# Performance work log

Measured on AMD Instinct MI355X. Metric: run time of the kernel, lower is better.

The kernel has to match this reference:

```python
import math
import jax, jax.numpy as jnp
import numpy as np

B, N, D = 2, 768, 512
H = 8
DK = D // H
BETA_NOT = 0.5
EPS = 1e-6


def setup_inputs() -> dict:
    key = jax.random.key(0)
    ks = jax.random.split(key, 8)
    s = 0.02
    return {
        "x": jax.random.normal(ks[0], (B, N, D), dtype=jnp.float32),
        "qkv1_w": jax.random.normal(ks[1], (D, 3 * D), dtype=jnp.float32) * s,
        "qkv2_w": jax.random.normal(ks[2], (D, 3 * D), dtype=jnp.float32) * s,
        "proj_w": jax.random.normal(ks[3], (D, D), dtype=jnp.float32) * s,
        "conv1_w": jax.random.normal(ks[4], (16, 6), dtype=jnp.float32) * 0.3,
        "conv1_b": jax.random.normal(ks[5], (16,), dtype=jnp.float32) * 0.1,
        "conv2_w": jax.random.normal(ks[6], (4, 16), dtype=jnp.float32) * 0.3,
        "conv2_b": jnp.full((4,), -5.0, dtype=jnp.float32),
        "chain_logit": jnp.asarray(-2.0, dtype=jnp.float32),
    }


def _qkv(x, w):
    b, n, d = x.shape
    qkv = (x @ w).reshape(b, n, 3, H, DK).transpose(2, 0, 3, 1, 4)  # [3,B,h,N,dk]
    return qkv[0], qkv[1], qkv[2]


def reference(x, qkv1_w, qkv2_w, proj_w, conv1_w, conv1_b, conv2_w, conv2_b, chain_logit):
    scale = 1.0 / math.sqrt(DK)
    q1, k1, v1 = _qkv(x, qkv1_w)
    q2, k2, v2 = _qkv(x, qkv2_w)

    S1 = jnp.einsum("bhnd,bhmd->bhnm", q1, k1) * scale  # [B,h,N,N]
    S2 = jnp.einsum("bhnd,bhmd->bhnm", q2, k2) * scale
    A1 = jax.nn.softmax(S1, axis=-1)
    A2 = jax.nn.softmax(S2, axis=-1)

    C_right = jnp.einsum("bhnk,bhkm->bhnm", A1, A2)
    C_left = jnp.einsum("bhnk,bhkm->bhnm", A2, A1)
    Cr = jnp.log(C_right + EPS)
    Cl = jnp.log(C_left + EPS)

    # 6-channel edge feature map [B,h,6,N,N]
    feat = jnp.stack(
        [S1, S2, jnp.swapaxes(S1, -1, -2), jnp.swapaxes(S2, -1, -2), Cr, Cl], axis=2
    )
    # 1x1 convs == per-pixel channel mixing
    hid = jnp.einsum("bhcnm,oc->bhonm", feat, conv1_w) + conv1_b[None, None, :, None, None]
    hid = jax.nn.gelu(hid, approximate=True)  # tanh-approx GELU
    gates = jax.nn.sigmoid(
        jnp.einsum("bhcnm,oc->bhonm", hid, conv2_w) + conv2_b[None, None, :, None, None]
    )
    g_and, g_or, g_not, g_chain = gates[:, :, 0], gates[:, :, 1], gates[:, :, 2], gates[:, :, 3]

    Smix = (
        S1
        + g_and * S2  # g_and * (S1 + S2 - S1)
        + g_or * (jnp.logaddexp(S1, S2) - S1)
        - g_not * (BETA_NOT * S2)
        + g_chain * Cr
    )
    A = jax.nn.softmax(Smix, axis=-1)

    y_base = jnp.einsum("bhnm,bhmd->bhnd", A, v1)
    transport = jnp.einsum("bhnm,bhmd->bhnd", A2, v2)
    y_chain = jnp.einsum("bhnm,bhmd->bhnd", A1, transport)
    w = jax.nn.sigmoid(chain_logit)
    y = y_base + w * y_chain

    y = jnp.swapaxes(y, 1, 2).reshape(x.shape[0], x.shape[1], D)  # [B,N,D]
    return y @ proj_w
```

## Files before the change

kernel.cpp:

```cpp
#include <hip/hip_runtime.h>
#include <hip/hip_bf16.h>
#include <math.h>

typedef __hip_bfloat16 bf16;
typedef __attribute__((ext_vector_type(8))) short short8;
typedef __attribute__((ext_vector_type(4))) float f32x4;
typedef __attribute__((ext_vector_type(2))) float f32x2;
#define DEVINL __device__ __forceinline__

constexpr int Bc  = 2;
constexpr int Nc  = 768;
constexpr int Dc  = 512;
constexpr int Hc  = 8;
constexpr int DKc = 64;
constexpr int BHc = Bc * Hc;
constexpr float SCALE    = 0.125f;
constexpr float EPSF     = 1e-6f;
constexpr float BETA_NOT = 0.5f;

DEVINL float ldf(const float* p, long i) { return p[i]; }
DEVINL float ldf(const bf16* p, long i) { return __bfloat162float(p[i]); }
DEVINL void stf(float* p, long i, float v) { p[i] = v; }
DEVINL void stf(bf16* p, long i, float v) { p[i] = __float2bfloat16(v); }

DEVINL float sigf(float x) { return __fdividef(1.f, 1.f + __expf(-x)); }

DEVINL f32x2 fma2(f32x2 a, f32x2 b, f32x2 c) { return __builtin_elementwise_fma(a, b, c); }
DEVINL f32x2 splat2(float x) { return (f32x2){x, x}; }
DEVINL float vexp2(float x) { float r; asm("v_exp_f32 %0, %1" : "=v"(r) : "v"(x)); return r; }
DEVINL float vrcp(float x)  { float r; asm("v_rcp_f32 %0, %1" : "=v"(r) : "v"(x)); return r; }
DEVINL float vlog2(float x) { float r; asm("v_log_f32 %0, %1" : "=v"(r) : "v"(x)); return r; }

DEVINL void gl_lds16(const void* g, void* l) {
    __builtin_amdgcn_global_load_lds(
        (const __attribute__((address_space(1))) void*)g,
        (__attribute__((address_space(3))) void*)l, 16, 0, 0);
}

DEVINL int sniff_is_fp32(const void* xraw) {
    const uint4* p4 = (const uint4*)xraw;
    float mx = 0.f;
#pragma unroll
    for (int j = 0; j < 16; ++j) {
        const uint4 u = p4[j];
        const unsigned w[4] = {u.x, u.y, u.z, u.w};
#pragma unroll
        for (int t = 0; t < 4; ++t) {
            mx = fmaxf(mx, fabsf(__uint_as_float((w[t] & 0xffffu) << 16)));
            mx = fmaxf(mx, fabsf(__uint_as_float(w[t] & 0xffff0000u)));
        }
    }
    return mx > 1000.f ? 1 : 0;
}

DEVINL float cvt_elem(const void* s, long j, int is32) {
    return is32 ? ((const float*)s)[j]
                : __bfloat162float(((const bf16*)s)[j]);
}

__global__ __launch_bounds__(256) void convert_tr(
    const void* x, const void* w1, const void* w2, const void* pw,
    const void* c1w, const void* c1b, const void* c2w, const void* c2b,
    const void* ch,
    bf16* xb, bf16* w1t, bf16* w2t, bf16* pwt, float* smallf)
{
    __shared__ unsigned short tile[64][68];
    __shared__ int is32s;
    if (threadIdx.x == 0) is32s = sniff_is_fp32(x);
    __syncthreads();
    const int is32 = is32s;
    const int t = blockIdx.x;
    const int tid = threadIdx.x;

    if (t < 448) {
        const void* src; bf16* dst; int R, C, bx, by;
        if (t < 192)      { src = w1; dst = w1t; R = Dc; C = 3 * Dc;
                            bx = t % 24;         by = t / 24; }
        else if (t < 384) { src = w2; dst = w2t; R = Dc; C = 3 * Dc;
                            bx = (t - 192) % 24; by = (t - 192) / 24; }
        else              { src = pw; dst = pwt; R = Dc; C = Dc;
                            bx = (t - 384) % 8;  by = (t - 384) / 8; }
        const int r0 = by * 64, c0 = bx * 64;
        const int lr = tid >> 4, lc4 = (tid & 15) * 4;
#pragma unroll
        for (int i = 0; i < 4; ++i) {
            const int r = lr + i * 16;
            const long base = (long)(r0 + r) * C + c0 + lc4;
            unsigned short v[4];
            if (is32) {
                const float4 f = *(const float4*)&((const float*)src)[base];
                const bf16 b0 = __float2bfloat16(f.x);
                const bf16 b1 = __float2bfloat16(f.y);
                const bf16 b2 = __float2bfloat16(f.z);
                const bf16 b3 = __float2bfloat16(f.w);
                v[0] = *(const unsigned short*)&b0;
                v[1] = *(const unsigned short*)&b1;
                v[2] = *(const unsigned short*)&b2;
                v[3] = *(const unsigned short*)&b3;
            } else {
                *(uint2*)v = *(const uint2*)&((const unsigned short*)src)[base];
            }
            *(uint2*)&tile[r][lc4] = *(const uint2*)v;
        }
        __syncthreads();
#pragma unroll
        for (int i = 0; i < 4; ++i) {
            const int r = lr + i * 16;
            unsigned short v[4];
#pragma unroll
            for (int j = 0; j < 4; ++j) v[j] = tile[lc4 + j][r];
            *(uint2*)&((unsigned short*)dst)[(long)(c0 + r) * R + r0 + lc4] =
                *(const uint2*)v;
        }
    } else if (t < 832) {
        const long i0 = (long)(t - 448) * 2048 + tid * 8;
        if (is32) {
            const float4 a = *(const float4*)&((const float*)x)[i0];
            const float4 b = *(const float4*)&((const float*)x)[i0 + 4];
            const float f[8] = {a.x, a.y, a.z, a.w, b.x, b.y, b.z, b.w};
            unsigned short o[8];
#pragma unroll
            for (int j = 0; j < 8; ++j) {
                const bf16 bb = __float2bfloat16(f[j]);
                o[j] = *(const unsigned short*)&bb;
            }
            *(uint4*)&((unsigned short*)xb)[i0] = *(const uint4*)o;
        } else {
            *(uint4*)&((unsigned short*)xb)[i0] =
                *(const uint4*)&((const unsigned short*)x)[i0];
        }
    } else {
#pragma unroll
        for (int base = 0; base < 512; base += 256) {
            const int i = base + tid;
            if (i < 384) {
                const int u = i / 24, k = i % 24;
                float v = 0.f;
                if (k < 12)      v = cvt_elem(c1w, u * 6 + (k >> 1), is32);
                else if (k < 14) v = cvt_elem(c1b, u, is32);
                else if (k >= 16) { const int o = (k - 16) >> 1;
                                    v = cvt_elem(c2w, o * 16 + u, is32); }
                smallf[i] = v;
            } else if (i < 392) smallf[i] = cvt_elem(c2b, (i - 384) >> 1, is32);
            else if (i < 394) smallf[i] = cvt_elem(ch, 0, is32);
            else smallf[i] = 0.f;
        }
    }
}

__global__ __launch_bounds__(256) void fill_sentinel(unsigned short* o) {
    const long i = (long)blockIdx.x * 256 + threadIdx.x;
    if (i < (long)Bc * Nc * Dc) o[i] = 0x40E0;
}

__global__ __launch_bounds__(256) void sgemm_softmax(
    const bf16* __restrict__ qg, const bf16* __restrict__ kg,
    float* __restrict__ Sg, bf16* __restrict__ Ag_, bf16* __restrict__ Atg)
{
    __shared__ unsigned short Bsm[256 * 72];
    __shared__ unsigned short Asm16[16 * 72];
    __shared__ float red[4][16];

    const int wg  = blockIdx.x;
    const int xcd = wg & 7, tt = wg >> 3;
    const int z   = xcd + 8 * (tt / 48);
    const int by  = tt % 48;
    const long MAT = (long)Nc * Nc;

    const bf16* Q  = qg + (long)z * (Nc * DKc) + (long)(by * 16) * DKc;
    const bf16* Km = kg + (long)z * (Nc * DKc);
    float* S  = Sg  + (long)z * MAT + (long)(by * 16) * Nc;
    bf16*  A  = Ag_ + (long)z * MAT + (long)(by * 16) * Nc;
    bf16*  At = Atg + (long)z * MAT;

    const int tid  = threadIdx.x;
    const int wv   = tid >> 6;
    const int lane = tid & 63;
    const int q    = lane >> 4;
    const int ln   = lane & 15;
    const int sr   = tid >> 3, k8 = tid & 7;

    if (tid < 128) {
        const int row = tid >> 3, kk = tid & 7;
        *(uint4*)&Asm16[row * 72 + kk * 8] = *(const uint4*)&Q[row * 64 + kk * 8];
    }

    f32x4 acc[12];
#pragma unroll
    for (int j = 0; j < 12; ++j) acc[j] = (f32x4){0.f, 0.f, 0.f, 0.f};

    for (int c = 0; c < 3; ++c) {
        __syncthreads();
#pragma unroll
        for (int i = 0; i < 8; ++i) {
            const int row = sr + i * 32;
            *(uint4*)&Bsm[row * 72 + k8 * 8] =
                *(const uint4*)&Km[(long)(c * 256 + row) * 64 + k8 * 8];
        }
        __syncthreads();
#pragma unroll
        for (int kc = 0; kc < 2; ++kc) {
            const short8 af = *(const short8*)&Asm16[ln * 72 + kc * 32 + q * 8];
#pragma unroll
            for (int t = 0; t < 4; ++t) {
                const int nl = wv * 64 + t * 16 + ln;
                const short8 bfr = *(const short8*)&Bsm[nl * 72 + kc * 32 + q * 8];
                acc[c * 4 + t] = __builtin_amdgcn_mfma_f32_16x16x32_bf16(
                    af, bfr, acc[c * 4 + t], 0, 0, 0);
            }
        }
    }

    float mrow[4] = {-1e30f, -1e30f, -1e30f, -1e30f};
#pragma unroll
    for (int j = 0; j < 12; ++j) {
        const int c = j >> 2, t = j & 3;
        const int col = c * 256 + wv * 64 + t * 16 + ln;
#pragma unroll
        for (int r = 0; r < 4; ++r) {
            const float v = acc[j][r] * SCALE;
            acc[j][r] = v;
            S[(long)(q * 4 + r) * Nc + col] = v;
            mrow[r] = fmaxf(mrow[r], v);
        }
    }
#pragma unroll
    for (int off = 8; off > 0; off >>= 1)
#pragma unroll
        for (int r = 0; r < 4; ++r)
            mrow[r] = fmaxf(mrow[r], __shfl_xor(mrow[r], off, 16));
    if (ln == 0)
#pragma unroll
        for (int r = 0; r < 4; ++r) red[wv][q * 4 + r] = mrow[r];
    __syncthreads();
    float m4[4];
#pragma unroll
    for (int r = 0; r < 4; ++r)
        m4[r] = fmaxf(fmaxf(red[0][q * 4 + r], red[1][q * 4 + r]),
                      fmaxf(red[2][q * 4 + r], red[3][q * 4 + r]));
    __syncthreads();

    float srow[4] = {0.f, 0.f, 0.f, 0.f};
#pragma unroll
    for (int j = 0; j < 12; ++j)
#pragma unroll
        for (int r = 0; r < 4; ++r) {
            const float e = __expf(acc[j][r] - m4[r]);
            acc[j][r] = e;
            srow[r] += e;
        }
#pragma unroll
    for (int off = 8; off > 0; off >>= 1)
#pragma unroll
        for (int r = 0; r < 4; ++r)
            srow[r] += __shfl_xor(srow[r], off, 16);
    if (ln == 0)
#pragma unroll
        for (int r = 0; r < 4; ++r) red[wv][q * 4 + r] = srow[r];
    __syncthreads();
    float inv[4];
#pragma unroll
    for (int r = 0; r < 4; ++r)
        inv[r] = 1.f / fmaxf(red[0][q * 4 + r] + red[1][q * 4 + r] +
                             red[2][q * 4 + r] + red[3][q * 4 + r], 1e-30f);

    unsigned short* ATl = Bsm;
#pragma unroll
    for (int j = 0; j < 12; ++j) {
        const int c = j >> 2, t = j & 3;
        const int col = c * 256 + wv * 64 + t * 16 + ln;
#pragma unroll
        for (int r = 0; r < 4; ++r) {
            const bf16 b = __float2bfloat16(acc[j][r] * inv[r]);
            const unsigned short u = *(const unsigned short*)&b;
            A[(long)(q * 4 + r) * Nc + col] = *(const bf16*)&u;
            ATl[col * 20 + q * 4 + r] = u;
        }
    }
    __syncthreads();
#pragma unroll
    for (int s = 0; s < 3; ++s) {
        const int m = tid + s * 256;
        uint2 v0 = *(const uint2*)&ATl[m * 20 + 0];
        uint2 v1 = *(const uint2*)&ATl[m * 20 + 4];
        uint2 v2 = *(const uint2*)&ATl[m * 20 + 8];
        uint2 v3 = *(const uint2*)&ATl[m * 20 + 12];
        unsigned short* d = (unsigned short*)&At[(long)m * Nc + by * 16];
        *(uint2*)&d[0]  = v0;
        *(uint2*)&d[4]  = v1;
        *(uint2*)&d[8]  = v2;
        *(uint2*)&d[12] = v3;
    }
}

template <int EPI, typename TC, int XORB = 0, int XCDSWZ = 0, int RAW = 0>
__global__ __launch_bounds__(256) void gemm_nt_mfma(
    const bf16* __restrict__ Ag, const bf16* __restrict__ Btg,
    TC* __restrict__ Cg, bf16* __restrict__ Craw, int M, int N, int K,
    long sA, long sB, long sC, float alpha)
{
    __shared__ unsigned short Asm[2 * 128 * 32];
    __shared__ unsigned short Bsm[2 * 128 * 32];
    constexpr int BUF = 128 * 32;

    int bx, by, bz;
    if (XCDSWZ) {
        const int wg = blockIdx.x;
        const int xcd = wg & 7, t = wg >> 3;
        bz = xcd + 8 * (t / 36);
        const int tile = t % 36;
        bx = tile % 6; by = tile / 6;
    } else { bx = blockIdx.x; by = blockIdx.y; bz = blockIdx.z; }

    const int tid  = threadIdx.x;
    const int wv   = tid >> 6;
    const int lane = tid & 63;
    const int q    = lane >> 4;
    const int ln   = lane & 15;
    const int wm   = wv & 1;
    const int wn   = wv >> 1;

    const int zb = XORB ? (bz ^ 16) : bz;
    const bf16* A  = Ag  + (long)bz * sA + (long)(by * 128) * K;
    const bf16* Bt = Btg + (long)zb * sB + (long)(bx * 128) * K;
    TC*         C  = Cg  + (long)bz * sC;

    const int sr = lane >> 2, sc = lane & 3;
    const int scs = sc ^ (sr & 3);
    const bf16* gA0 = A  + (long)(wv * 32 + sr)      * K + scs * 8;
    const bf16* gA1 = A  + (long)(wv * 32 + 16 + sr) * K + scs * 8;
    const bf16* gB0 = Bt + (long)(wv * 32 + sr)      * K + scs * 8;
    const bf16* gB1 = Bt + (long)(wv * 32 + 16 + sr) * K + scs * 8;
    unsigned short* lA0 = &Asm[(wv * 32)      * 32];
    unsigned short* lA1 = &Asm[(wv * 32 + 16) * 32];
    unsigned short* lB0 = &Bsm[(wv * 32)      * 32];
    unsigned short* lB1 = &Bsm[(wv * 32 + 16) * 32];

    f32x4 acc[4][4];
#pragma unroll
    for (int i = 0; i < 4; ++i)
#pragma unroll
        for (int j = 0; j < 4; ++j)
            acc[i][j] = (f32x4){0.f, 0.f, 0.f, 0.f};

    const int qs = (q ^ (ln & 3)) * 8;

    gl_lds16(gA0, lA0);
    gl_lds16(gA1, lA1);
    gl_lds16(gB0, lB0);
    gl_lds16(gB1, lB1);
    __syncthreads();

    int cur = 0;
    for (int k0 = 0; k0 < K; k0 += 32) {
        const int nxt = cur ^ 1;
        if (k0 + 32 < K) {
            const int no = nxt * BUF;
            gl_lds16(gA0 + k0 + 32, lA0 + no);
            gl_lds16(gA1 + k0 + 32, lA1 + no);
            gl_lds16(gB0 + k0 + 32, lB0 + no);
            gl_lds16(gB1 + k0 + 32, lB1 + no);
        }

        const unsigned short* Ac = &Asm[cur * BUF];
        const unsigned short* Bc = &Bsm[cur * BUF];
        short8 af[4], bfr[4];
#pragma unroll
        for (int mt = 0; mt < 4; ++mt) {
            int m = wm * 64 + mt * 16 + ln;
            af[mt] = *(const short8*)&Ac[m * 32 + qs];
        }
#pragma unroll
        for (int nt = 0; nt < 4; ++nt) {
            int n = wn * 64 + nt * 16 + ln;
            bfr[nt] = *(const short8*)&Bc[n * 32 + qs];
        }
#pragma unroll
        for (int mt = 0; mt < 4; ++mt)
#pragma unroll
            for (int nt = 0; nt < 4; ++nt)
                acc[mt][nt] = __builtin_amdgcn_mfma_f32_16x16x32_bf16(
                    af[mt], bfr[nt], acc[mt][nt], 0, 0, 0);

        __syncthreads();
        cur = nxt;
    }

#pragma unroll
    for (int mt = 0; mt < 4; ++mt) {
#pragma unroll
        for (int nt = 0; nt < 4; ++nt) {
            const int col = bx * 128 + wn * 64 + nt * 16 + ln;
            const int rowb = by * 128 + wm * 64 + mt * 16 + q * 4;
#pragma unroll
            for (int r = 0; r < 4; ++r) {
                float vraw = acc[mt][nt][r] * alpha;
                if (RAW) {
                    if (bz < 16)
                        Craw[(long)bz * M * N + (long)(rowb + r) * N + col] =
                            __float2bfloat16(vraw);
                }
                float v = vraw;
                if (EPI == 1) v = __logf(fmaxf(v, 0.f) + EPSF);
                stf(C, (long)(rowb + r) * N + col, v);
            }
        }
    }
}

__global__ __launch_bounds__(256) void qkv_mfma64(
    const bf16* __restrict__ X,
    const bf16* __restrict__ w1t, const bf16* __restrict__ w2t,
    bf16* __restrict__ q1, bf16* __restrict__ k1, bf16* __restrict__ v1t,
    bf16* __restrict__ q2, bf16* __restrict__ k2, bf16* __restrict__ v2t)
{
    constexpr int K = Dc;
    __shared__ unsigned short Asm[2 * 64 * 32];
    __shared__ unsigned short Bsm[2 * 128 * 32];
    constexpr int ABUF = 64 * 32, BBUF = 128 * 32;

    const int tid  = threadIdx.x;
    const int wv   = tid >> 6;
    const int lane = tid & 63;
    const int q    = lane >> 4;
    const int ln   = lane & 15;
    const int wm   = wv & 1;
    const int wn   = wv >> 1;
    const int set  = blockIdx.z;

    const bf16* Wt = set ? w2t : w1t;
    bf16* Q  = set ? q2 : q1;
    bf16* Ko = set ? k2 : k1;
    bf16* Vt = set ? v2t : v1t;

    const bf16* A  = X  + (long)(blockIdx.y * 64) * K;
    const bf16* Bt = Wt + (long)(blockIdx.x * 128) * K;

    const int sr = lane >> 2, sc = lane & 3;
    const int scs = sc ^ (sr & 3);
    const bf16* gA0 = A  + (long)(wv * 16 + sr)      * K + scs * 8;
    const bf16* gB0 = Bt + (long)(wv * 32 + sr)      * K + scs * 8;
    const bf16* gB1 = Bt + (long)(wv * 32 + 16 + sr) * K + scs * 8;
    unsigned short* lA0 = &Asm[(wv * 16)      * 32];
    unsigned short* lB0 = &Bsm[(wv * 32)      * 32];
    unsigned short* lB1 = &Bsm[(wv * 32 + 16) * 32];

    f32x4 acc[2][4];
#pragma unroll
    for (int i = 0; i < 2; ++i)
#pragma unroll
        for (int j = 0; j < 4; ++j)
            acc[i][j] = (f32x4){0.f, 0.f, 0.f, 0.f};

    const int qs = (q ^ (ln & 3)) * 8;

    gl_lds16(gA0, lA0);
    gl_lds16(gB0, lB0);
    gl_lds16(gB1, lB1);
    __syncthreads();

    int cur = 0;
    for (int k0 = 0; k0 < K; k0 += 32) {
        const int nxt = cur ^ 1;
        if (k0 + 32 < K) {
            gl_lds16(gA0 + k0 + 32, lA0 + nxt * ABUF);
            gl_lds16(gB0 + k0 + 32, lB0 + nxt * BBUF);
            gl_lds16(gB1 + k0 + 32, lB1 + nxt * BBUF);
        }

        const unsigned short* Ac = &Asm[cur * ABUF];
        const unsigned short* Bc = &Bsm[cur * BBUF];
        short8 af[2], bfr[4];
#pragma unroll
        for (int mt = 0; mt < 2; ++mt) {
            int m = wm * 32 + mt * 16 + ln;
            af[mt] = *(const short8*)&Ac[m * 32 + qs];
        }
#pragma unroll
        for (int nt = 0; nt < 4; ++nt) {
            int n = wn * 64 + nt * 16 + ln;
            bfr[nt] = *(const short8*)&Bc[n * 32 + qs];
        }
#pragma unroll
        for (int mt = 0; mt < 2; ++mt)
#pragma unroll
            for (int nt = 0; nt < 4; ++nt)
                acc[mt][nt] = __builtin_amdgcn_mfma_f32_16x16x32_bf16(
                    af[mt], bfr[nt], acc[mt][nt], 0, 0, 0);

        __syncthreads();
        cur = nxt;
    }

#pragma unroll
    for (int mt = 0; mt < 2; ++mt) {
#pragma unroll
        for (int nt = 0; nt < 4; ++nt) {
            const int col  = blockIdx.x * 128 + wn * 64 + nt * 16 + ln;
            const int rowb = blockIdx.y * 64 + wm * 32 + mt * 16 + q * 4;
            const int t = col >> 9;
            const int h = (col >> 6) & 7;
            const int dk = col & 63;
            if (t == 2) {
                const int b = rowb >= Nc ? 1 : 0;
                const int n = rowb - b * Nc;
                unsigned short o[4];
#pragma unroll
                for (int r = 0; r < 4; ++r) {
                    const bf16 bb = __float2bfloat16(acc[mt][nt][r]);
                    o[r] = *(const unsigned short*)&bb;
                }
                unsigned short* d = (unsigned short*)Vt +
                    (((long)b * Hc + h) * DKc + dk) * Nc + n;
                *(uint2*)d = *(const uint2*)o;
            } else {
                bf16* dst = (t == 0) ? Q : Ko;
#pragma unroll
                for (int r = 0; r < 4; ++r) {
                    const int row = rowb + r;
                    const int b = row >= Nc ? 1 : 0;
                    const int n = row - b * Nc;
                    dst[(((long)b * Hc + h) * Nc + n) * DKc + dk] =
                        __float2bfloat16(acc[mt][nt][r]);
                }
            }
        }
    }
}

struct N64Acc { f32x4 acc[2][4]; };

template <typename DUMMY = void>
DEVINL void n64_core(const bf16* A, const bf16* Bt, int K,
                     unsigned short* Asm, unsigned short* Bsm, N64Acc& R)
{
    const int tid  = threadIdx.x;
    const int wave = tid >> 6;
    const int lane = tid & 63;
    const int q    = lane >> 4;
    const int ln   = lane & 15;

    const int sr = tid >> 3, k8 = tid & 7;
    const bf16* pa[4];
    const bf16* pb[2];
    int wa[4], wb[2];
#pragma unroll
    for (int i = 0; i < 4; ++i) {
        pa[i] = A + (long)(sr + i * 32) * K + k8 * 8;
        wa[i] = (sr + i * 32) * 72 + k8 * 8;
    }
#pragma unroll
    for (int i = 0; i < 2; ++i) {
        pb[i] = Bt + (long)(sr + i * 32) * K + k8 * 8;
        wb[i] = (sr + i * 32) * 72 + k8 * 8;
    }

#pragma unroll
    for (int i = 0; i < 2; ++i)
#pragma unroll
        for (int j = 0; j < 4; ++j)
            R.acc[i][j] = (f32x4){0.f, 0.f, 0.f, 0.f};

    for (int k0 = 0; k0 < K; k0 += 64) {
        uint4 va[4], vb[2];
#pragma unroll
        for (int i = 0; i < 4; ++i) va[i] = *(const uint4*)(pa[i] + k0);
#pragma unroll
        for (int i = 0; i < 2; ++i) vb[i] = *(const uint4*)(pb[i] + k0);
        __syncthreads();
#pragma unroll
        for (int i = 0; i < 4; ++i) *(uint4*)&Asm[wa[i]] = va[i];
#pragma unroll
        for (int i = 0; i < 2; ++i) *(uint4*)&Bsm[wb[i]] = vb[i];
        __syncthreads();

#pragma unroll
        for (int kc = 0; kc < 2; ++kc) {
            short8 af[2], bfr[4];
#pragma unroll
            for (int mt = 0; mt < 2; ++mt) {
                int m = wave * 32 + mt * 16 + ln;
                af[mt] = *(const short8*)&Asm[m * 72 + kc * 32 + q * 8];
            }
#pragma unroll
            for (int nt = 0; nt < 4; ++nt) {
                int n = nt * 16 + ln;
                bfr[nt] = *(const short8*)&Bsm[n * 72 + kc * 32 + q * 8];
            }
#pragma unroll
            for (int mt = 0; mt < 2; ++mt)
#pragma unroll
                for (int nt = 0; nt < 4; ++nt)
                    R.acc[mt][nt] = __builtin_amdgcn_mfma_f32_16x16x32_bf16(
                        af[mt], bfr[nt], R.acc[mt][nt], 0, 0, 0);
        }
    }
}

struct N64hAcc { f32x4 acc[4]; };

template <typename DUMMY = void>
DEVINL void n64h_core(const bf16* A, const bf16* Bt, int K,
                      unsigned short* Asm, unsigned short* Bsm, N64hAcc& R)
{
    const int tid  = threadIdx.x;
    const int wave = tid >> 6;
    const int lane = tid & 63;
    const int q    = lane >> 4;
    const int ln   = lane & 15;

    const int sr = tid >> 3, k8 = tid & 7;
    const bf16* pa[2];
    const bf16* pb[2];
    int wa[2], wb[2];
#pragma unroll
    for (int i = 0; i < 2; ++i) {
        pa[i] = A  + (long)(sr + i * 32) * K + k8 * 8;
        wa[i] = (sr + i * 32) * 72 + k8 * 8;
        pb[i] = Bt + (long)(sr + i * 32) * K + k8 * 8;
        wb[i] = wa[i];
    }

#pragma unroll
    for (int j = 0; j < 4; ++j)
        R.acc[j] = (f32x4){0.f, 0.f, 0.f, 0.f};

    for (int k0 = 0; k0 < K; k0 += 64) {
        uint4 va[2], vb[2];
#pragma unroll
        for (int i = 0; i < 2; ++i) va[i] = *(const uint4*)(pa[i] + k0);
#pragma unroll
        for (int i = 0; i < 2; ++i) vb[i] = *(const uint4*)(pb[i] + k0);
        __syncthreads();
#pragma unroll
        for (int i = 0; i < 2; ++i) *(uint4*)&Asm[wa[i]] = va[i];
#pragma unroll
        for (int i = 0; i < 2; ++i) *(uint4*)&Bsm[wb[i]] = vb[i];
        __syncthreads();

#pragma unroll
        for (int kc = 0; kc < 2; ++kc) {
            short8 af;
            af = *(const short8*)&Asm[(wave * 16 + ln) * 72 + kc * 32 + q * 8];
            short8 bfr[4];
#pragma unroll
            for (int nt = 0; nt < 4; ++nt) {
                int n = nt * 16 + ln;
                bfr[nt] = *(const short8*)&Bsm[n * 72 + kc * 32 + q * 8];
            }
#pragma unroll
            for (int nt = 0; nt < 4; ++nt)
                R.acc[nt] = __builtin_amdgcn_mfma_f32_16x16x32_bf16(
                    af, bfr[nt], R.acc[nt], 0, 0, 0);
        }
    }
}

__global__ __launch_bounds__(256) void gemm_n64_pair(
    const bf16* __restrict__ A0g, const bf16* __restrict__ B0g, bf16* __restrict__ C0tg,
    const bf16* __restrict__ A1g, const bf16* __restrict__ B1g, bf16* __restrict__ C1g,
    int M, int K, long sA, long sB, long sC)
{
    __shared__ unsigned short Asm[128 * 72];
    __shared__ unsigned short Bsm[64 * 72];

    const int zz = blockIdx.z & 15;
    const int second = blockIdx.z >> 4;
    const bf16* A  = (second ? A1g : A0g) + (long)zz * sA + (long)(blockIdx.y * 128) * K;
    const bf16* Bt = (second ? B1g : B0g) + (long)zz * sB;

    N64Acc R;
    n64_core(A, Bt, K, Asm, Bsm, R);

    const int tid = threadIdx.x;
    const int wave = tid >> 6, lane = tid & 63, q = lane >> 4, ln = lane & 15;

    if (second) {
        bf16* C = C1g + (long)zz * sC;
#pragma unroll
        for (int mt = 0; mt < 2; ++mt) {
#pragma unroll
            for (int nt = 0; nt < 4; ++nt) {
                const int col  = nt * 16 + ln;
                const int rowb = blockIdx.y * 128 + wave * 32 + mt * 16 + q * 4;
#pragma unroll
                for (int r = 0; r < 4; ++r)
                    C[(long)(rowb + r) * 64 + col] = __float2bfloat16(R.acc[mt][nt][r]);
            }
        }
    } else {
        __syncthreads();
#pragma unroll
        for (int mt = 0; mt < 2; ++mt) {
#pragma unroll
            for (int nt = 0; nt < 4; ++nt) {
                const int col = nt * 16 + ln;
                const int rwb = wave * 32 + mt * 16 + q * 4;
#pragma unroll
                for (int r = 0; r < 4; ++r)
                    *(bf16*)&Asm[col * 136 + rwb + r] = __float2bfloat16(R.acc[mt][nt][r]);
            }
        }
        __syncthreads();
        bf16* Ct = C0tg + (long)zz * sC;
        const int dk  = tid >> 2;
        const int nc0 = (tid & 3) * 32;
        const int gn0 = blockIdx.y * 128;
#pragma unroll
        for (int c8 = 0; c8 < 4; ++c8) {
            uint4 v = *(const uint4*)&Asm[dk * 136 + nc0 + c8 * 8];
            *(uint4*)&Ct[(long)dk * Nc + gn0 + nc0 + c8 * 8] = v;
        }
    }
}

__global__ __launch_bounds__(256) void gemm_n64_both_h(
    const bf16* __restrict__ Ab, const bf16* __restrict__ v1t,
    const bf16* __restrict__ Craw, const bf16* __restrict__ v2t,
    const float* __restrict__ smallf, bf16* __restrict__ yc,
    int K, long sA, long sB)
{
    __shared__ unsigned short Asm[64 * 72];
    __shared__ unsigned short Bsm[64 * 72];

    const int bh = blockIdx.z;
    const long arow = (long)(blockIdx.y * 64) * K;

    N64hAcc R1;
    n64h_core(Ab + (long)bh * sA + arow, v1t + (long)bh * sB, K, Asm, Bsm, R1);
    N64hAcc R2;
    n64h_core(Craw + (long)bh * sA + arow, v2t + (long)bh * sB, K, Asm, Bsm, R2);

    const float w = sigf(smallf[392]);
    const int b = bh >> 3, h = bh & 7;

    const int tid = threadIdx.x;
    const int wave = tid >> 6, lane = tid & 63, q = lane >> 4, ln = lane & 15;
#pragma unroll
    for (int nt = 0; nt < 4; ++nt) {
        const int col  = nt * 16 + ln;
        const int rowb = blockIdx.y * 64 + wave * 16 + q * 4;
#pragma unroll
        for (int r = 0; r < 4; ++r) {
            const int n = rowb + r;
            yc[((long)(b * Nc + n)) * Dc + h * DKc + col] =
                __float2bfloat16(R1.acc[nt][r] + w * R2.acc[nt][r]);
        }
    }
}

__global__ __launch_bounds__(256) void gemm_n64_combine(
    const bf16* __restrict__ A1b, const bf16* __restrict__ trt,
    const bf16* __restrict__ yb1, const float* __restrict__ smallf,
    bf16* __restrict__ yc, int M, int K, long sA, long sB)
{
    __shared__ unsigned short Asm[128 * 72];
    __shared__ unsigned short Bsm[64 * 72];

    const int bh = blockIdx.z;
    const bf16* A  = A1b + (long)bh * sA + (long)(blockIdx.y * 128) * K;
    const bf16* Bt = trt + (long)bh * sB;

    N64Acc R;
    n64_core(A, Bt, K, Asm, Bsm, R);

    const float w = sigf(smallf[392]);
    const int b = bh >> 3, h = bh & 7;
    const long yb1base = (long)bh * Nc * DKc;

    const int tid = threadIdx.x;
    const int wave = tid >> 6, lane = tid & 63, q = lane >> 4, ln = lane & 15;
#pragma unroll
    for (int mt = 0; mt < 2; ++mt) {
#pragma unroll
        for (int nt = 0; nt < 4; ++nt) {
            const int col  = nt * 16 + ln;
            const int rowb = blockIdx.y * 128 + wave * 32 + mt * 16 + q * 4;
#pragma unroll
            for (int r = 0; r < 4; ++r) {
                const int n = rowb + r;
                const float base = __bfloat162float(yb1[yb1base + (long)n * 64 + col]);
                yc[((long)(b * Nc + n)) * Dc + h * DKc + col] =
                    __float2bfloat16(base + w * R.acc[mt][nt][r]);
            }
        }
    }
}

__global__ __launch_bounds__(256) void gemm_n64_yb(
    const bf16* __restrict__ Ag, const bf16* __restrict__ Btg,
    bf16* __restrict__ Cg, int M, int K, long sA, long sB, long sC)
{
    __shared__ unsigned short Asm[128 * 72];
    __shared__ unsigned short Bsm[64 * 72];

    const int zz = blockIdx.z;
    const bf16* A  = Ag + (long)zz * sA + (long)(blockIdx.y * 128) * K;
    const bf16* Bt = Btg + (long)zz * sB;

    N64Acc R;
    n64_core(A, Bt, K, Asm, Bsm, R);

    bf16* C = Cg + (long)zz * sC;
    const int tid = threadIdx.x;
    const int wave = tid >> 6, lane = tid & 63, q = lane >> 4, ln = lane & 15;
#pragma unroll
    for (int mt = 0; mt < 2; ++mt) {
#pragma unroll
        for (int nt = 0; nt < 4; ++nt) {
            const int col  = nt * 16 + ln;
            const int rowb = blockIdx.y * 128 + wave * 32 + mt * 16 + q * 4;
#pragma unroll
            for (int r = 0; r < 4; ++r)
                C[(long)(rowb + r) * 64 + col] = __float2bfloat16(R.acc[mt][nt][r]);
        }
    }
}

__global__ __launch_bounds__(256) void softmax_rows_w(
    const float* __restrict__ src, bf16* __restrict__ dst)
{
    const int wid  = threadIdx.x >> 6;
    const int lane = threadIdx.x & 63;
    const long row = (long)blockIdx.x * 4 + wid;
    const float* s = src + row * Nc;

    float4 v[3];
#pragma unroll
    for (int i = 0; i < 3; ++i)
        v[i] = *(const float4*)&s[i * 256 + lane * 4];

    float m = -1e30f;
#pragma unroll
    for (int i = 0; i < 3; ++i)
        m = fmaxf(m, fmaxf(fmaxf(v[i].x, v[i].y), fmaxf(v[i].z, v[i].w)));
#pragma unroll
    for (int off = 32; off > 0; off >>= 1)
        m = fmaxf(m, __shfl_xor(m, off, 64));

    float e[12];
    float sum = 0.f;
#pragma unroll
    for (int i = 0; i < 3; ++i) {
        e[i * 4 + 0] = __expf(v[i].x - m);
        e[i * 4 + 1] = __expf(v[i].y - m);
        e[i * 4 + 2] = __expf(v[i].z - m);
        e[i * 4 + 3] = __expf(v[i].w - m);
        sum += e[i * 4 + 0] + e[i * 4 + 1] + e[i * 4 + 2] + e[i * 4 + 3];
    }
#pragma unroll
    for (int off = 32; off > 0; off >>= 1)
        sum += __shfl_xor(sum, off, 64);

    const float inv = 1.f / fmaxf(sum, 1e-30f);
    unsigned short* d = (unsigned short*)dst + row * Nc;
#pragma unroll
    for (int i = 0; i < 3; ++i) {
        unsigned short o[4];
#pragma unroll
        for (int j = 0; j < 4; ++j) {
            const bf16 b = __float2bfloat16(e[i * 4 + j] * inv);
            o[j] = *(const unsigned short*)&b;
        }
        *(uint2*)&d[i * 256 + lane * 4] = *(const uint2*)o;
    }
}

__global__ __launch_bounds__(256) void gates_smix(
    const float* __restrict__ S1g, const float* __restrict__ S2g,
    const bf16* __restrict__ Crg, const bf16* __restrict__ Clg,
    float* __restrict__ Smixg, const float* __restrict__ smallf)
{
    __shared__ float t1t[32][17], t2t[32][17];

    const long mat = (long)blockIdx.z * Nc * Nc;
    const float* S1 = S1g + mat;
    const float* S2 = S2g + mat;
    const unsigned short* Cr = (const unsigned short*)Crg + mat;
    const unsigned short* Cl = (const unsigned short*)Clg + mat;
    float* Smix = Smixg + mat;

    const int tid = threadIdx.x;

    const int n0 = blockIdx.y * 16, m0 = blockIdx.x * 32;
    {
        const int r = tid >> 3, c2 = (tid & 7) * 2;
        const float2 a = *(const float2*)&S1[(long)(m0 + r) * Nc + n0 + c2];
        const float2 b = *(const float2*)&S2[(long)(m0 + r) * Nc + n0 + c2];
        t1t[r][c2] = a.x; t1t[r][c2 + 1] = a.y;
        t2t[r][c2] = b.x; t2t[r][c2 + 1] = b.y;
    }
    __syncthreads();

    const int tx = tid & 15, ty = tid >> 4;
    const int n = n0 + ty;
    const long idx = (long)n * Nc + m0 + tx * 2;

    const float2 s1v = *(const float2*)&S1[idx];
    const float2 s2v = *(const float2*)&S2[idx];
    const unsigned cru = *(const unsigned*)&Cr[idx];
    const unsigned clu = *(const unsigned*)&Cl[idx];

    const f32x2 s1a = {s1v.x, s1v.y};
    const f32x2 s2a = {s2v.x, s2v.y};
    const f32x2 cra = {__uint_as_float((cru & 0xffffu) << 16),
                       __uint_as_float(cru & 0xffff0000u)};
    const f32x2 cla = {__uint_as_float((clu & 0xffffu) << 16),
                       __uint_as_float(clu & 0xffff0000u)};
    const f32x2 s1t = {t1t[tx * 2][ty], t1t[tx * 2 + 1][ty]};
    const f32x2 s2t = {t2t[tx * 2][ty], t2t[tx * 2 + 1][ty]};

    f32x2 g0 = *(const f32x2*)&smallf[384];
    f32x2 g1 = *(const f32x2*)&smallf[386];
    f32x2 g2 = *(const f32x2*)&smallf[388];
    f32x2 g3 = *(const f32x2*)&smallf[390];

    const f32x2 gc1  = splat2(-2.30220902f);
    const f32x2 gc3  = splat2(-0.10294357f);
    const f32x2 one2 = splat2(1.f);

#pragma unroll
    for (int u = 0; u < 16; ++u) {
        const f32x2* cw = (const f32x2*)&smallf[u * 24];
        f32x2 h = cw[6];
        h = fma2(s1a, cw[0], h);
        h = fma2(s2a, cw[1], h);
        h = fma2(s1t, cw[2], h);
        h = fma2(s2t, cw[3], h);
        h = fma2(cra, cw[4], h);
        h = fma2(cla, cw[5], h);
        const f32x2 hh = h * h;
        const f32x2 z2 = h * fma2(hh, gc3, gc1);
        f32x2 e;  e[0]  = vexp2(z2[0]); e[1]  = vexp2(z2[1]);
        const f32x2 d = one2 + e;
        f32x2 rc; rc[0] = vrcp(d[0]);   rc[1] = vrcp(d[1]);
        const f32x2 hid = h * rc;
        g0 = fma2(hid, cw[8],  g0);
        g1 = fma2(hid, cw[9],  g1);
        g2 = fma2(hid, cw[10], g2);
        g3 = fma2(hid, cw[11], g3);
    }

    const f32x2 nl2e = splat2(-1.44269504f);
    const f32x2 ln2v = splat2(0.69314718f);
    auto sig2 = [&](f32x2 x) -> f32x2 {
        const f32x2 t = x * nl2e;
        f32x2 e;  e[0] = vexp2(t[0]); e[1] = vexp2(t[1]);
        const f32x2 d = one2 + e;
        f32x2 r;  r[0] = vrcp(d[0]);  r[1] = vrcp(d[1]);
        return r;
    };
    const f32x2 ga2 = sig2(g0);
    const f32x2 go2 = sig2(g1);
    const f32x2 gn2 = sig2(g2);
    const f32x2 gc2 = sig2(g3);

    const f32x2 dd = s1a - s2a;
    f32x2 ad; ad[0] = fabsf(dd[0]); ad[1] = fabsf(dd[1]);
    const f32x2 t2 = ad * nl2e;
    f32x2 ee; ee[0] = vexp2(t2[0]); ee[1] = vexp2(t2[1]);
    const f32x2 lp = one2 + ee;
    f32x2 lg; lg[0] = vlog2(lp[0]); lg[1] = vlog2(lp[1]);
    const f32x2 mx2 = __builtin_elementwise_max(s1a, s2a);
    const f32x2 lae = fma2(lg, ln2v, mx2);

    f32x2 o2 = s1a;
    o2 = fma2(ga2, s2a, o2);
    o2 = fma2(go2, lae - s1a, o2);
    o2 = fma2(gn2, s2a * splat2(-BETA_NOT), o2);
    o2 = fma2(gc2, cra, o2);
    *(float2*)&Smix[idx] = (float2){o2[0], o2[1]};
}

__global__ __launch_bounds__(256) void proj_n64h(
    const bf16* __restrict__ yc, const bf16* __restrict__ pwt,
    const void* __restrict__ xraw, void* __restrict__ out)
{
    constexpr int K = Dc;
    constexpr int N = Dc;
    __shared__ unsigned short Asm[64 * 72];
    __shared__ unsigned short Bsm[64 * 72];
    __shared__ int is32s;
    if (threadIdx.x == 0) is32s = sniff_is_fp32(xraw);

    const bf16* A  = yc  + (long)(blockIdx.y * 64) * K;
    const bf16* Bt = pwt + (long)(blockIdx.x * 64) * K;

    N64hAcc R;
    n64h_core(A, Bt, K, Asm, Bsm, R);

    const int is32 = is32s;
    const int tid = threadIdx.x;
    const int wave = tid >> 6, lane = tid & 63, q = lane >> 4, ln = lane & 15;
#pragma unroll
    for (int nt = 0; nt < 4; ++nt) {
        const int col  = blockIdx.x * 64 + nt * 16 + ln;
        const int rowb = blockIdx.y * 64 + wave * 16 + q * 4;
#pragma unroll
        for (int r = 0; r < 4; ++r) {
            const long o = (long)(rowb + r) * N + col;
            if (is32) ((float*)out)[o] = R.acc[nt][r];
            else      ((bf16*)out)[o] = __float2bfloat16(R.acc[nt][r]);
        }
    }
}

extern "C" void kernel_launch(void* const* d_in, const int* in_sizes, int n_in,
                              void* d_out, int out_size, void* d_ws, size_t ws_size,
                              hipStream_t stream)
{
    const size_t HD   = (size_t)BHc * Nc * DKc;
    const size_t HDh  = HD / 2;
    const size_t MAT  = (size_t)Nc * Nc;
    const size_t MATS = (size_t)BHc * MAT;
    const long   HSTR = (long)Nc * DKc;

    float* ws = (float*)d_ws;
    size_t off = 0;
    auto alloc = [&](size_t n) { float* p = ws + off; off += n; return p; };

    bf16* xb  = (bf16*)alloc(HDh);
    bf16* w1t = (bf16*)alloc(HDh);
    bf16* w2t = (bf16*)alloc(HDh);
    bf16* pwt = (bf16*)alloc((size_t)Dc * Dc / 2);
    float* smallf = alloc(512);
    bf16* q1b = (bf16*)alloc(HDh); bf16* q2b = (bf16*)alloc(HDh);
    bf16* k1b = (bf16*)alloc(HDh); bf16* k2b = (bf16*)alloc(HDh);
    bf16* v1t = (bf16*)alloc(HDh); bf16* v2t = (bf16*)alloc(HDh);
    bf16* trt = (bf16*)alloc(HDh);
    float* S1   = alloc(MATS);
    float* S2   = alloc(MATS);
    float* Smix = alloc(MATS);
    bf16* A1b = (bf16*)alloc(MATS / 2);
    bf16* A2b = (bf16*)alloc(MATS / 2);
    bf16* Crb = (bf16*)alloc(MATS / 2);
    bf16* Clb = (bf16*)alloc(MATS / 2);
    bf16* yb1 = (bf16*)alloc(HDh);
    bf16* yc  = (bf16*)alloc(HDh);

    const size_t NEED_BASE = off * sizeof(float);
    bf16* Crawb = (bf16*)alloc(MATS / 2);
    const size_t NEED_A = off * sizeof(float);
    const int pathA = ws_size >= NEED_A;

    bf16* A1tb = (bf16*)Smix;
    bf16* A2tb = ((bf16*)Smix) + MATS;
    bf16* Ab   = (bf16*)S1;

    if (ws_size < NEED_BASE) {
        fill_sentinel<<<dim3(3072), 256, 0, stream>>>((unsigned short*)d_out);
        return;
    }

    convert_tr<<<dim3(833), 256, 0, stream>>>(
        d_in[0], d_in[1], d_in[2], d_in[3], d_in[4], d_in[5], d_in[6], d_in[7],
        d_in[8], xb, w1t, w2t, pwt, smallf);
    qkv_mfma64<<<dim3(12, 24, 2), 256, 0, stream>>>(
        xb, w1t, w2t, q1b, k1b, v1t, q2b, k2b, v2t);

    sgemm_softmax<<<dim3(1536), 256, 0, stream>>>(
        q1b, k1b, S1, A1b, A1tb);

    if (pathA)
        gemm_nt_mfma<1, bf16, 1, 1, 1><<<dim3(1152), 256, 0, stream>>>(
            A1b, A1tb, Crb, Crawb, Nc, Nc, Nc, (long)MAT, (long)MAT, (long)MAT, 1.f);
    else
        gemm_nt_mfma<1, bf16, 1, 1, 0><<<dim3(1152), 256, 0, stream>>>(
            A1b, A1tb, Crb, nullptr, Nc, Nc, Nc, (long)MAT, (long)MAT, (long)MAT, 1.f);

    gates_smix<<<dim3(24, 48, BHc), 256, 0, stream>>>(S1, S2, Crb, Clb, Smix, smallf);

    softmax_rows_w<<<(BHc * Nc) / 4, 256, 0, stream>>>(Smix, Ab);

    if (pathA) {
        gemm_n64_both_h<<<dim3(1, 12, BHc), 256, 0, stream>>>(
            Ab, v1t, Crawb, v2t, smallf, yc, Nc, (long)MAT, HSTR);
    } else {
        gemm_n64_pair<<<dim3(1, 6, 2 * BHc), 256, 0, stream>>>(
            A2b, v2t, trt, Ab, v1t, yb1, Nc, Nc, (long)MAT, HSTR, HSTR);
        gemm_n64_combine<<<dim3(1, 6, BHc), 256, 0, stream>>>(
            A1b, trt, yb1, smallf, yc, Nc, Nc, (long)MAT, HSTR);
    }

    proj_n64h<<<dim3(8, 24, 1), 256, 0, stream>>>(yc, pwt, d_in[0], d_out);
}
```

Before: 325.5 us.

## Fuse final softmax into the A·V1 + chain GEMM kernel on pathA

The separate row-softmax kernel, which wrote bf16 probabilities for Smix, is replaced on pathA by a fused GEMM kernel. The kernel first computes per-row max and sum over its 64 rows, then exponentiates and normalises fp32 Smix tiles on the fly while staging them into shared memory for the MFMA product with v1. This removes one launch and the bf16 probability write and re-read. In exchange, each block reads Smix twice in fp32 (once for the stats, once for the GEMM), does more exp work inside a low-occupancy 192-block grid, and the stats pass is serial per wave.

```diff
diff --git a/kernel.cpp b/kernel.cpp
--- a/kernel.cpp
+++ b/kernel.cpp
@@ -656,6 +656,135 @@
     }
 }
 
+__global__ __launch_bounds__(256) void gemm_n64_both_sm(
+    const float* __restrict__ Smixg, const bf16* __restrict__ v1t,
+    const bf16* __restrict__ Craw, const bf16* __restrict__ v2t,
+    const float* __restrict__ smallf, bf16* __restrict__ yc,
+    long sA, long sB)
+{
+    __shared__ unsigned short Asm[64 * 72];
+    __shared__ unsigned short Bsm[64 * 72];
+    __shared__ float mrow[64], irow[64];
+
+    const int bh = blockIdx.z;
+    const int by = blockIdx.y;
+    const float* Sx = Smixg + (long)bh * (Nc * Nc) + (long)(by * 64) * Nc;
+
+    const int tid  = threadIdx.x;
+    const int wave = tid >> 6;
+    const int lane = tid & 63;
+    const int q    = lane >> 4;
+    const int ln   = lane & 15;
+
+    for (int rr = 0; rr < 16; ++rr) {
+        const int row = wave * 16 + rr;
+        const float* s = &Sx[(long)row * Nc];
+        float4 v[3];
+#pragma unroll
+        for (int i = 0; i < 3; ++i)
+            v[i] = *(const float4*)&s[i * 256 + lane * 4];
+        float m = -1e30f;
+#pragma unroll
+        for (int i = 0; i < 3; ++i)
+            m = fmaxf(m, fmaxf(fmaxf(v[i].x, v[i].y), fmaxf(v[i].z, v[i].w)));
+#pragma unroll
+        for (int off = 32; off > 0; off >>= 1)
+            m = fmaxf(m, __shfl_xor(m, off, 64));
+        float sum = 0.f;
+#pragma unroll
+        for (int i = 0; i < 3; ++i) {
+            sum += __expf(v[i].x - m) + __expf(v[i].y - m) +
+                   __expf(v[i].z - m) + __expf(v[i].w - m);
+        }
+#pragma unroll
+        for (int off = 32; off > 0; off >>= 1)
+            sum += __shfl_xor(sum, off, 64);
+        if (lane == 0) {
+            mrow[row] = m;
+            irow[row] = 1.f / fmaxf(sum, 1e-30f);
+        }
+    }
+    __syncthreads();
+
+    const int sr = tid >> 3, k8 = tid & 7;
+    const bf16* BtV = v1t + (long)bh * sB;
+    const bf16* pb[2];
+    int wz[2];
+#pragma unroll
+    for (int i = 0; i < 2; ++i) {
+        pb[i] = BtV + (long)(sr + i * 32) * Nc + k8 * 8;
+        wz[i] = (sr + i * 32) * 72 + k8 * 8;
+    }
+
+    N64hAcc R1;
+#pragma unroll
+    for (int j = 0; j < 4; ++j) R1.acc[j] = (f32x4){0.f, 0.f, 0.f, 0.f};
+
+    for (int k0 = 0; k0 < Nc; k0 += 64) {
+        float4 xa[2][2];
+        uint4 vb[2];
+#pragma unroll
+        for (int i = 0; i < 2; ++i) {
+            const long base = (long)(sr + i * 32) * Nc + k0 + k8 * 8;
+            xa[i][0] = *(const float4*)&Sx[base];
+            xa[i][1] = *(const float4*)&Sx[base + 4];
+        }
+#pragma unroll
+        for (int i = 0; i < 2; ++i) vb[i] = *(const uint4*)(pb[i] + k0);
+        __syncthreads();
+#pragma unroll
+        for (int i = 0; i < 2; ++i) {
+            const int row = sr + i * 32;
+            const float m = mrow[row], iv = irow[row];
+            const float* xf = (const float*)&xa[i][0];
+            unsigned short o[8];
+#pragma unroll
+            for (int j = 0; j < 8; ++j) {
+                const bf16 bb = __float2bfloat16(__expf(xf[j] - m) * iv);
+                o[j] = *(const unsigned short*)&bb;
+            }
+            *(uint4*)&Asm[wz[i]] = *(const uint4*)o;
+        }
+#pragma unroll
+        for (int i = 0; i < 2; ++i) *(uint4*)&Bsm[wz[i]] = vb[i];
+        __syncthreads();
+
+#pragma unroll
+        for (int kc = 0; kc < 2; ++kc) {
+            const short8 af =
+                *(const short8*)&Asm[(wave * 16 + ln) * 72 + kc * 32 + q * 8];
+            short8 bfr[4];
+#pragma unroll
+            for (int nt = 0; nt < 4; ++nt) {
+                int n = nt * 16 + ln;
+                bfr[nt] = *(const short8*)&Bsm[n * 72 + kc * 32 + q * 8];
+            }
+#pragma unroll
+            for (int nt = 0; nt < 4; ++nt)
+                R1.acc[nt] = __builtin_amdgcn_mfma_f32_16x16x32_bf16(
+                    af, bfr[nt], R1.acc[nt], 0, 0, 0);
+        }
+    }
+
+    N64hAcc R2;
+    n64h_core(Craw + (long)bh * sA + (long)(by * 64) * Nc,
+              v2t + (long)bh * sB, Nc, Asm, Bsm, R2);
+
+    const float w = sigf(smallf[392]);
+    const int b = bh >> 3, h = bh & 7;
+#pragma unroll
+    for (int nt = 0; nt < 4; ++nt) {
+        const int col  = nt * 16 + ln;
+        const int rowb = by * 64 + wave * 16 + q * 4;
+#pragma unroll
+        for (int r = 0; r < 4; ++r) {
+            const int n = rowb + r;
+            yc[((long)(b * Nc + n)) * Dc + h * DKc + col] =
+                __float2bfloat16(R1.acc[nt][r] + w * R2.acc[nt][r]);
+        }
+    }
+}
+
 __global__ __launch_bounds__(256) void gemm_n64_pair(
     const bf16* __restrict__ A0g, const bf16* __restrict__ B0g, bf16* __restrict__ C0tg,
     const bf16* __restrict__ A1g, const bf16* __restrict__ B1g, bf16* __restrict__ C1g,
@@ -710,41 +839,6 @@
         for (int c8 = 0; c8 < 4; ++c8) {
             uint4 v = *(const uint4*)&Asm[dk * 136 + nc0 + c8 * 8];
             *(uint4*)&Ct[(long)dk * Nc + gn0 + nc0 + c8 * 8] = v;
-        }
-    }
-}
-
-__global__ __launch_bounds__(256) void gemm_n64_both_h(
-    const bf16* __restrict__ Ab, const bf16* __restrict__ v1t,
-    const bf16* __restrict__ Craw, const bf16* __restrict__ v2t,
-    const float* __restrict__ smallf, bf16* __restrict__ yc,
-    int K, long sA, long sB)
-{
-    __shared__ unsigned short Asm[64 * 72];
-    __shared__ unsigned short Bsm[64 * 72];
-
-    const int bh = blockIdx.z;
-    const long arow = (long)(blockIdx.y * 64) * K;
-
-    N64hAcc R1;
-    n64h_core(Ab + (long)bh * sA + arow, v1t + (long)bh * sB, K, Asm, Bsm, R1);
-    N64hAcc R2;
-    n64h_core(Craw + (long)bh * sA + arow, v2t + (long)bh * sB, K, Asm, Bsm, R2);
-
-    const float w = sigf(smallf[392]);
-    const int b = bh >> 3, h = bh & 7;
-
-    const int tid = threadIdx.x;
-    const int wave = tid >> 6, lane = tid & 63, q = lane >> 4, ln = lane & 15;
-#pragma unroll
-    for (int nt = 0; nt < 4; ++nt) {
-        const int col  = nt * 16 + ln;
-        const int rowb = blockIdx.y * 64 + wave * 16 + q * 4;
-#pragma unroll
-        for (int r = 0; r < 4; ++r) {
-            const int n = rowb + r;
-            yc[((long)(b * Nc + n)) * Dc + h * DKc + col] =
-                __float2bfloat16(R1.acc[nt][r] + w * R2.acc[nt][r]);
         }
     }
 }
@@ -1070,12 +1164,11 @@
 
     gates_smix<<<dim3(24, 48, BHc), 256, 0, stream>>>(S1, S2, Crb, Clb, Smix, smallf);
 
-    softmax_rows_w<<<(BHc * Nc) / 4, 256, 0, stream>>>(Smix, Ab);
-
     if (pathA) {
-        gemm_n64_both_h<<<dim3(1, 12, BHc), 256, 0, stream>>>(
-            Ab, v1t, Crawb, v2t, smallf, yc, Nc, (long)MAT, HSTR);
+        gemm_n64_both_sm<<<dim3(1, 12, BHc), 256, 0, stream>>>(
+            Smix, v1t, Crawb, v2t, smallf, yc, (long)MAT, HSTR);
     } else {
+        softmax_rows_w<<<(BHc * Nc) / 4, 256, 0, stream>>>(Smix, Ab);
         gemm_n64_pair<<<dim3(1, 6, 2 * BHc), 256, 0, stream>>>(
             A2b, v2t, trt, Ab, v1t, yb1, Nc, Nc, (long)MAT, HSTR, HSTR);
         gemm_n64_combine<<<dim3(1, 6, BHc), 256, 0, stream>>>(
```

Result: faster. 309.8 us (-4.8%).
